# Kernel tuning notes

Measured on AMD Instinct MI355X. Metric: run time of the kernel, lower is better.

## Reference

```python
import jax, jax.numpy as jnp
import numpy as np

D_MODEL, D_STATE, D_CONV, D_INNER, DT_RANK = 96, 16, 3, 192, 6
BATCH, H, W = 4, 64, 64


def setup_inputs() -> dict:
    key = jax.random.key(0)
    ks = jax.random.split(key, 8)
    s = 0.02
    return {
        "x": jax.random.normal(ks[0], (BATCH, H, W, D_MODEL), jnp.float32),
        "in_proj_w": jax.random.normal(ks[1], (2 * D_INNER, D_MODEL), jnp.float32) * s,
        "conv_w": jax.random.normal(ks[2], (D_INNER, 1, D_CONV, D_CONV), jnp.float32) * s,
        "conv_b": jnp.zeros((D_INNER,), jnp.float32),
        "x_proj_w": jax.random.normal(ks[3], (4, DT_RANK + 2 * D_STATE, D_INNER), jnp.float32) * s,
        "dt_w": jax.random.normal(ks[4], (4, D_INNER, DT_RANK), jnp.float32) * s,
        # dt bias ~ inverse-softplus of dt in [1e-3, 1e-1] (roughly log-uniform negative values)
        "dt_b": jax.random.uniform(ks[5], (4, D_INNER), jnp.float32, minval=-6.0, maxval=-2.3),
        "A_logs": jnp.log(jnp.tile(jnp.arange(1, D_STATE + 1, dtype=jnp.float32), (4 * D_INNER, 1))),
        "Ds": jnp.ones((4 * D_INNER,), jnp.float32),
        "ln_w": jnp.ones((D_INNER,), jnp.float32),
        "ln_b": jnp.zeros((D_INNER,), jnp.float32),
        "out_proj_w": jax.random.normal(ks[6], (D_MODEL, D_INNER), jnp.float32) * s,
    }


def _ss2d(x, in_proj_w, conv_w, conv_b, x_proj_w, dt_w, dt_b, A_logs, Ds, ln_w, ln_b, out_proj_w):
    B, Hh, Ww, C = x.shape
    D = conv_w.shape[0]          # d_inner
    N = A_logs.shape[1]          # d_state
    R = dt_w.shape[2]            # dt_rank
    L = Hh * Ww
    K = 4

    xz = x @ in_proj_w.T                          # (B,H,W,2D)
    xi, z = jnp.split(xz, 2, axis=-1)
    xc = jnp.transpose(xi, (0, 3, 1, 2))          # (B,D,H,W)
    pad = (D_CONV - 1) // 2
    xc = jax.lax.conv_general_dilated(xc, conv_w, (1, 1), ((pad, pad), (pad, pad)),
                                      feature_group_count=D)
    xc = jax.nn.silu(xc + conv_b[None, :, None, None])

    # 4 scan directions: row-major, col-major, and their reverses
    x_flat = xc.reshape(B, D, L)
    x_tr = jnp.transpose(xc, (0, 1, 3, 2)).reshape(B, D, L)
    x_hwwh = jnp.stack([x_flat, x_tr], axis=1)                     # (B,2,D,L)
    xs = jnp.concatenate([x_hwwh, jnp.flip(x_hwwh, axis=-1)], axis=1)  # (B,K,D,L)

    x_dbl = jnp.einsum('bkdl,kcd->bkcl', xs, x_proj_w)
    dts, Bs, Cs = jnp.split(x_dbl, [R, R + N], axis=2)             # (B,K,R,L),(B,K,N,L),(B,K,N,L)
    dts = jnp.einsum('bkrl,kdr->bkdl', dts, dt_w)
    delta = jax.nn.softplus(dts + dt_b[None, :, :, None])          # (B,K,D,L)
    A = -jnp.exp(A_logs).reshape(K, D, N)                          # (K,D,N)

    # sequential selective scan over L (L-first for lax.scan)
    u_seq = jnp.moveaxis(xs, -1, 0)        # (L,B,K,D)
    dt_seq = jnp.moveaxis(delta, -1, 0)    # (L,B,K,D)
    B_seq = jnp.moveaxis(Bs, -1, 0)        # (L,B,K,N)
    C_seq = jnp.moveaxis(Cs, -1, 0)        # (L,B,K,N)

    def step(h, inp):
        u_t, dt_t, B_t, C_t = inp
        h = jnp.exp(dt_t[..., None] * A) * h + (dt_t * u_t)[..., None] * B_t[:, :, None, :]
        y = jnp.einsum('bkdn,bkn->bkd', h, C_t)
        return h, y

    h0 = jnp.zeros((B, K, D, N), jnp.float32)
    _, ys = jax.lax.scan(step, h0, (u_seq, dt_seq, B_seq, C_seq))
    out_y = jnp.moveaxis(ys, 0, -1) + Ds.reshape(K, D)[None, :, :, None] * xs  # (B,K,D,L)

    y1 = out_y[:, 0]
    y2 = jnp.transpose(out_y[:, 1].reshape(B, D, Ww, Hh), (0, 1, 3, 2)).reshape(B, D, L)
    y3 = jnp.flip(out_y[:, 2], axis=-1)
    y4 = jnp.transpose(jnp.flip(out_y[:, 3], axis=-1).reshape(B, D, Ww, Hh), (0, 1, 3, 2)).reshape(B, D, L)
    y = y1 + y2 + y3 + y4                                           # (B,D,L)

    y = jnp.transpose(y, (0, 2, 1)).reshape(B, Hh, Ww, D)
    mu = y.mean(-1, keepdims=True)
    var = y.var(-1, keepdims=True)
    y = (y - mu) * jax.lax.rsqrt(var + 1e-5) * ln_w + ln_b
    y = y * jax.nn.silu(z)
    return y @ out_proj_w.T


def reference(x, in_proj_w, conv_w, conv_b, x_proj_w, dt_w, dt_b, A_logs, Ds, ln_w, ln_b, out_proj_w):
    return _ss2d(x, in_proj_w, conv_w, conv_b, x_proj_w, dt_w, dt_b, A_logs, Ds, ln_w, ln_b, out_proj_w)
```

## Files before the change

### kernel.cpp

```cpp
#include <hip/hip_runtime.h>

constexpr int BATCH = 4;
constexpr int HS    = 64;
constexpr int WSZ   = 64;
constexpr int LSEQ  = 4096;
constexpr int DM    = 96;
constexpr int DI    = 192;
constexpr int NS    = 16;
constexpr int RK    = 6;
constexpr int KD    = 4;
constexpr int NCH   = 128;
constexpr int CLEN  = 32;
constexpr int XDS   = 160;

__device__ __forceinline__ int pos_of(int k, int l) {
  switch (k & 3) {
    case 0: return l;
    case 1: return ((l & 63) << 6) | (l >> 6);
    case 2: return LSEQ - 1 - l;
    default: { int lp = LSEQ - 1 - l; return ((lp & 63) << 6) | (lp >> 6); }
  }
}

__device__ __forceinline__ float softplus_f(float s) {
  return (s > 20.f) ? s : __logf(1.f + __expf(s));
}

__launch_bounds__(256)
__global__ void transpose_w(const float* __restrict__ in, float* __restrict__ outp,
                            int R, int C_) {
  int idx = blockIdx.x * 256 + threadIdx.x;
  if (idx < R * C_) {
    int r = idx / C_, c = idx % C_;
    outp[(size_t)c * R + r] = in[idx];
  }
}

template <int NN, int KK, int TM, int KT>
__launch_bounds__(256)
__global__ void gemm_nt(const float* __restrict__ A, const float* __restrict__ BT,
                        float* __restrict__ C, int M) {
  constexpr int TN  = 64;
  constexpr int RPT = TM / 16;
  constexpr int SA  = KT + 4;
  constexpr int KQ  = KT / 4;
  __shared__ float As[TM][SA];
  __shared__ float Bs[KT][TN];
  const int t = threadIdx.x;
  const int row0 = blockIdx.y * TM;
  const int col0 = blockIdx.x * TN;
  const int tc = t & 15;
  const int tr = t >> 4;

  float acc[RPT][4];
  #pragma unroll
  for (int i = 0; i < RPT; ++i)
    { acc[i][0]=0.f; acc[i][1]=0.f; acc[i][2]=0.f; acc[i][3]=0.f; }

  for (int k0 = 0; k0 < KK; k0 += KT) {
    #pragma unroll 1
    for (int idx = t; idx < TM * KQ; idx += 256) {
      int r = idx / KQ, kq = idx % KQ;
      *(float4*)&As[r][kq * 4] =
          *(const float4*)&A[(size_t)(row0 + r) * KK + k0 + kq * 4];
    }
    #pragma unroll 1
    for (int idx = t; idx < KT * 16; idx += 256) {
      int kk = idx >> 4, cq = idx & 15;
      int col = col0 + cq * 4;
      float4 v = make_float4(0.f, 0.f, 0.f, 0.f);
      if (col < NN) v = *(const float4*)&BT[(size_t)(k0 + kk) * NN + col];
      *(float4*)&Bs[kk][cq * 4] = v;
    }
    __syncthreads();
    #pragma unroll 4
    for (int kk = 0; kk < KT; ++kk) {
      float4 bv = *(const float4*)&Bs[kk][tc * 4];
      #pragma unroll
      for (int i = 0; i < RPT; ++i) {
        float a = As[tr * RPT + i][kk];
        acc[i][0] += a * bv.x; acc[i][1] += a * bv.y;
        acc[i][2] += a * bv.z; acc[i][3] += a * bv.w;
      }
    }
    __syncthreads();
  }
  int c = col0 + tc * 4;
  if (c < NN) {
    #pragma unroll
    for (int i = 0; i < RPT; ++i) {
      size_t r0 = (size_t)(row0 + tr * RPT + i) * NN + c;
      *(float4*)&C[r0] = make_float4(acc[i][0], acc[i][1], acc[i][2], acc[i][3]);
    }
  }
}

__launch_bounds__(256)
__global__ void conv_silu(const float* __restrict__ xz, const float* __restrict__ cw,
                          const float* __restrict__ cb, float* __restrict__ xc) {
  int idx = blockIdx.x * 256 + threadIdx.x;
  int d = idx % DI;
  int p = (idx / DI) % LSEQ;
  int b = idx / (DI * LSEQ);
  int h = p >> 6, w = p & 63;
  float acc = cb[d];
  #pragma unroll
  for (int kh = 0; kh < 3; ++kh) {
    int hh = h + kh - 1;
    if ((unsigned)hh >= (unsigned)HS) continue;
    #pragma unroll
    for (int kw = 0; kw < 3; ++kw) {
      int ww = w + kw - 1;
      if ((unsigned)ww >= (unsigned)WSZ) continue;
      acc += xz[((size_t)b * LSEQ + (hh << 6) + ww) * (2 * DI) + d] * cw[d * 9 + kh * 3 + kw];
    }
  }
  xc[idx] = acc / (1.f + __expf(-acc));
}

__launch_bounds__(256)
__global__ void build_wcatT(const float* __restrict__ xw, float* __restrict__ WcatT) {
  int idx = blockIdx.x * 256 + threadIdx.x;
  int col = idx / XDS, j = idx % XDS;
  int k = j / 40, jj = j % 40;
  float v = 0.f;
  int src = -1;
  if (jj < 16)      src = k * 38 + 6 + jj;
  else if (jj < 32) src = k * 38 + 22 + (jj - 16);
  else if (jj < 38) src = k * 38 + (jj - 32);
  if (src >= 0) v = xw[(size_t)src * DI + col];
  WcatT[idx] = v;
}

__launch_bounds__(192)
__global__ void scan_phase1(const float* __restrict__ xc, const float* __restrict__ xdbl,
                            const float* __restrict__ Alog, const float* __restrict__ dtw,
                            const float* __restrict__ dtb,
                            float* __restrict__ hN, float* __restrict__ sumdB) {
  const int d = threadIdx.x;
  const int ch = blockIdx.x, k = blockIdx.y, b = blockIdx.z;
  const int bk = b * KD + k;
  __shared__ float4 Bsh[CLEN * 6];
  {
    int idx = d;
    int j = idx / 6, q = idx % 6;
    int p = pos_of(k, ch * CLEN + j);
    int qq = (q < 4) ? q : (q + 4);
    Bsh[idx] = *(const float4*)&xdbl[(size_t)(b * LSEQ + p) * XDS + k * 40 + qq * 4];
  }
  float An[NS];
  {
    const float4* Ap = (const float4*)&Alog[((size_t)k * DI + d) * NS];
    #pragma unroll
    for (int q = 0; q < 4; ++q) {
      float4 a = Ap[q];
      An[q*4+0] = -__expf(a.x); An[q*4+1] = -__expf(a.y);
      An[q*4+2] = -__expf(a.z); An[q*4+3] = -__expf(a.w);
    }
  }
  float w[RK];
  #pragma unroll
  for (int r = 0; r < RK; ++r) w[r] = dtw[((size_t)k * DI + d) * RK + r];
  const float bsv = dtb[k * DI + d];
  const float An0 = An[0];
  bool geo = true;
  #pragma unroll
  for (int n = 0; n < NS; ++n)
    geo = geo && (fabsf(An[n] - (n + 1) * An0) <= 1e-3f * fabsf(An[n]));
  __syncthreads();

  float h[NS];
  #pragma unroll
  for (int n = 0; n < NS; ++n) h[n] = 0.f;
  float sumd = 0.f;
  const int l0 = ch * CLEN;
  if (geo) {
    #pragma unroll 2
    for (int j = 0; j < CLEN; ++j) {
      const int p = pos_of(k, l0 + j);
      const size_t bp = (size_t)b * LSEQ + p;
      float4 t0 = Bsh[j * 6 + 4], t1 = Bsh[j * 6 + 5];
      float s = bsv + w[0]*t0.x + w[1]*t0.y + w[2]*t0.z + w[3]*t0.w + w[4]*t1.x + w[5]*t1.y;
      float dl = softplus_f(s);
      float du = dl * xc[bp * DI + d];
      float we = __expf(dl * An0), wp = 1.f;
      #pragma unroll
      for (int q = 0; q < 4; ++q) {
        float4 v = Bsh[j * 6 + q];
        wp *= we; h[q*4+0] = wp * h[q*4+0] + du * v.x;
        wp *= we; h[q*4+1] = wp * h[q*4+1] + du * v.y;
        wp *= we; h[q*4+2] = wp * h[q*4+2] + du * v.z;
        wp *= we; h[q*4+3] = wp * h[q*4+3] + du * v.w;
      }
      sumd += dl;
    }
  } else {
    #pragma unroll 1
    for (int j = 0; j < CLEN; ++j) {
      const int p = pos_of(k, l0 + j);
      const size_t bp = (size_t)b * LSEQ + p;
      float4 t0 = Bsh[j * 6 + 4], t1 = Bsh[j * 6 + 5];
      float s = bsv + w[0]*t0.x + w[1]*t0.y + w[2]*t0.z + w[3]*t0.w + w[4]*t1.x + w[5]*t1.y;
      float dl = softplus_f(s);
      float du = dl * xc[bp * DI + d];
      #pragma unroll
      for (int q = 0; q < 4; ++q) {
        float4 v = Bsh[j * 6 + q];
        h[q*4+0] = __expf(dl * An[q*4+0]) * h[q*4+0] + du * v.x;
        h[q*4+1] = __expf(dl * An[q*4+1]) * h[q*4+1] + du * v.y;
        h[q*4+2] = __expf(dl * An[q*4+2]) * h[q*4+2] + du * v.z;
        h[q*4+3] = __expf(dl * An[q*4+3]) * h[q*4+3] + du * v.w;
      }
      sumd += dl;
    }
  }
  const size_t o = ((size_t)bk * NCH + ch) * DI + d;
  float4* Hp = (float4*)&hN[o * NS];
  #pragma unroll
  for (int q = 0; q < 4; ++q)
    Hp[q] = make_float4(h[q*4+0], h[q*4+1], h[q*4+2], h[q*4+3]);
  sumdB[o] = sumd;
}

__launch_bounds__(256)
__global__ void chunk_combine(float* __restrict__ hN, const float* __restrict__ sumdB,
                              const float* __restrict__ Alog) {
  const int tid = blockIdx.x * 256 + threadIdx.x;
  const int n  = tid & 15;
  const int dd = tid >> 4;
  const int d  = dd % DI;
  const int bk = dd / DI;
  const int k  = bk & 3;
  const float An = -__expf(Alog[((size_t)k * DI + d) * NS + n]);
  float h = 0.f;
  #pragma unroll 1
  for (int c = 0; c < NCH; ++c) {
    const size_t o = ((size_t)bk * NCH + c) * DI + d;
    float tmp = hN[o * NS + n];
    hN[o * NS + n] = h;
    h = tmp + __expf(An * sumdB[o]) * h;
  }
}

__launch_bounds__(192)
__global__ void scan_phase2(const float* __restrict__ xc, const float* __restrict__ xdbl,
                            const float* __restrict__ Alog, const float* __restrict__ dtw,
                            const float* __restrict__ dtb, const float* __restrict__ hin,
                            float* __restrict__ yg) {
  const int d = threadIdx.x;
  const int ch = blockIdx.x, k = blockIdx.y, b = blockIdx.z;
  const int bk = b * KD + k;
  __shared__ float4 Bsh[CLEN * 10];
  #pragma unroll 1
  for (int idx = d; idx < CLEN * 10; idx += 192) {
    int j = idx / 10, q = idx % 10;
    int p = pos_of(k, ch * CLEN + j);
    Bsh[idx] = *(const float4*)&xdbl[(size_t)(b * LSEQ + p) * XDS + k * 40 + q * 4];
  }
  float An[NS];
  {
    const float4* Ap = (const float4*)&Alog[((size_t)k * DI + d) * NS];
    #pragma unroll
    for (int q = 0; q < 4; ++q) {
      float4 a = Ap[q];
      An[q*4+0] = -__expf(a.x); An[q*4+1] = -__expf(a.y);
      An[q*4+2] = -__expf(a.z); An[q*4+3] = -__expf(a.w);
    }
  }
  float w[RK];
  #pragma unroll
  for (int r = 0; r < RK; ++r) w[r] = dtw[((size_t)k * DI + d) * RK + r];
  const float bsv = dtb[k * DI + d];
  const float An0 = An[0];
  bool geo = true;
  #pragma unroll
  for (int n = 0; n < NS; ++n)
    geo = geo && (fabsf(An[n] - (n + 1) * An0) <= 1e-3f * fabsf(An[n]));

  float h[NS];
  {
    const size_t o = ((size_t)bk * NCH + ch) * DI + d;
    const float4* Hp = (const float4*)&hin[o * NS];
    #pragma unroll
    for (int q = 0; q < 4; ++q) {
      float4 v = Hp[q];
      h[q*4+0] = v.x; h[q*4+1] = v.y; h[q*4+2] = v.z; h[q*4+3] = v.w;
    }
  }
  __syncthreads();
  const int l0 = ch * CLEN;
  if (geo) {
    #pragma unroll 2
    for (int j = 0; j < CLEN; ++j) {
      const int p = pos_of(k, l0 + j);
      const size_t bp = (size_t)b * LSEQ + p;
      float4 t0 = Bsh[j * 10 + 8], t1 = Bsh[j * 10 + 9];
      float s = bsv + w[0]*t0.x + w[1]*t0.y + w[2]*t0.z + w[3]*t0.w + w[4]*t1.x + w[5]*t1.y;
      float dl = softplus_f(s);
      float du = dl * xc[bp * DI + d];
      float we = __expf(dl * An0), wp = 1.f;
      float y = 0.f;
      #pragma unroll
      for (int q = 0; q < 4; ++q) {
        float4 v  = Bsh[j * 10 + q];
        float4 c4 = Bsh[j * 10 + 4 + q];
        wp *= we; h[q*4+0] = wp * h[q*4+0] + du * v.x; y += h[q*4+0] * c4.x;
        wp *= we; h[q*4+1] = wp * h[q*4+1] + du * v.y; y += h[q*4+1] * c4.y;
        wp *= we; h[q*4+2] = wp * h[q*4+2] + du * v.z; y += h[q*4+2] * c4.z;
        wp *= we; h[q*4+3] = wp * h[q*4+3] + du * v.w; y += h[q*4+3] * c4.w;
      }
      atomicAdd(&yg[bp * DI + d], y);
    }
  } else {
    #pragma unroll 1
    for (int j = 0; j < CLEN; ++j) {
      const int p = pos_of(k, l0 + j);
      const size_t bp = (size_t)b * LSEQ + p;
      float4 t0 = Bsh[j * 10 + 8], t1 = Bsh[j * 10 + 9];
      float s = bsv + w[0]*t0.x + w[1]*t0.y + w[2]*t0.z + w[3]*t0.w + w[4]*t1.x + w[5]*t1.y;
      float dl = softplus_f(s);
      float du = dl * xc[bp * DI + d];
      float y = 0.f;
      #pragma unroll
      for (int q = 0; q < 4; ++q) {
        float4 v  = Bsh[j * 10 + q];
        float4 c4 = Bsh[j * 10 + 4 + q];
        h[q*4+0] = __expf(dl * An[q*4+0]) * h[q*4+0] + du * v.x; y += h[q*4+0] * c4.x;
        h[q*4+1] = __expf(dl * An[q*4+1]) * h[q*4+1] + du * v.y; y += h[q*4+1] * c4.y;
        h[q*4+2] = __expf(dl * An[q*4+2]) * h[q*4+2] + du * v.z; y += h[q*4+2] * c4.z;
        h[q*4+3] = __expf(dl * An[q*4+3]) * h[q*4+3] + du * v.w; y += h[q*4+3] * c4.w;
      }
      atomicAdd(&yg[bp * DI + d], y);
    }
  }
}

__launch_bounds__(192)
__global__ void fuse_ln(const float* __restrict__ yg, const float* __restrict__ xc,
                        const float* __restrict__ Ds, const float* __restrict__ xz,
                        const float* __restrict__ lnw, const float* __restrict__ lnb,
                        float* __restrict__ ymul) {
  const int row = blockIdx.x;
  const int d = threadIdx.x;
  float u = xc[(size_t)row * DI + d];
  float sDs = Ds[d] + Ds[DI + d] + Ds[2 * DI + d] + Ds[3 * DI + d];
  float y = yg[(size_t)row * DI + d] + sDs * u;
  float s1 = y, s2 = y * y;
  #pragma unroll
  for (int off = 32; off; off >>= 1) {
    s1 += __shfl_xor(s1, off);
    s2 += __shfl_xor(s2, off);
  }
  __shared__ float r1[3], r2[3];
  int wid = d >> 6;
  if ((d & 63) == 0) { r1[wid] = s1; r2[wid] = s2; }
  __syncthreads();
  float S1 = r1[0] + r1[1] + r1[2];
  float S2 = r2[0] + r2[1] + r2[2];
  float mu = S1 * (1.f / DI);
  float var = S2 * (1.f / DI) - mu * mu;
  float yn = (y - mu) * rsqrtf(var + 1e-5f) * lnw[d] + lnb[d];
  float zv = xz[(size_t)row * (2 * DI) + DI + d];
  float g = zv / (1.f + __expf(-zv));
  ymul[(size_t)row * DI + d] = yn * g;
}

extern "C" void kernel_launch(void* const* d_in, const int* in_sizes, int n_in,
                              void* d_out, int out_size, void* d_ws, size_t ws_size,
                              hipStream_t stream) {
  (void)in_sizes; (void)n_in; (void)out_size; (void)ws_size;
  const float* x          = (const float*)d_in[0];
  const float* in_proj_w  = (const float*)d_in[1];
  const float* conv_w     = (const float*)d_in[2];
  const float* conv_b     = (const float*)d_in[3];
  const float* x_proj_w   = (const float*)d_in[4];
  const float* dt_w       = (const float*)d_in[5];
  const float* dt_b       = (const float*)d_in[6];
  const float* A_logs     = (const float*)d_in[7];
  const float* Ds         = (const float*)d_in[8];
  const float* ln_w       = (const float*)d_in[9];
  const float* ln_b       = (const float*)d_in[10];
  const float* out_proj_w = (const float*)d_in[11];
  float* out = (float*)d_out;
  float* ws  = (float*)d_ws;

  constexpr size_t SZ_XZ    = (size_t)BATCH * LSEQ * 2 * DI;
  constexpr size_t SZ_XC    = (size_t)BATCH * LSEQ * DI;
  constexpr size_t SZ_XD    = (size_t)BATCH * LSEQ * XDS;
  constexpr size_t SZ_HN    = (size_t)BATCH * KD * NCH * DI * NS;
  constexpr size_t SZ_SUMD  = (size_t)BATCH * KD * NCH * DI;

  float* xz    = ws;
  float* xc    = xz + SZ_XZ;
  float* xdbl  = xc + SZ_XC;
  float* hN    = xdbl + SZ_XD;
  float* sumd  = hN + SZ_HN;
  float* yg    = sumd + SZ_SUMD;
  float* ymul  = yg + SZ_XC;
  float* WcatT = ymul + SZ_XC;
  float* inpT  = WcatT + (size_t)DI * XDS;
  float* outpT = inpT + (size_t)DM * 2 * DI;

  const int M = BATCH * LSEQ;

  build_wcatT<<<(DI * XDS) / 256, 256, 0, stream>>>(x_proj_w, WcatT);
  transpose_w<<<(2 * DI * DM + 255) / 256, 256, 0, stream>>>(in_proj_w, inpT, 2 * DI, DM);
  transpose_w<<<(DM * DI + 255) / 256, 256, 0, stream>>>(out_proj_w, outpT, DM, DI);
  gemm_nt<2 * DI, DM, 64, 96><<<dim3(6, M / 64), 256, 0, stream>>>(x, inpT, xz, M);
  conv_silu<<<(BATCH * LSEQ * DI) / 256, 256, 0, stream>>>(xz, conv_w, conv_b, xc);
  gemm_nt<XDS, DI, 64, 96><<<dim3(3, M / 64), 256, 0, stream>>>(xc, WcatT, xdbl, M);
  scan_phase1<<<dim3(NCH, KD, BATCH), 192, 0, stream>>>(xc, xdbl, A_logs, dt_w, dt_b,
                                                        hN, sumd);
  chunk_combine<<<(BATCH * KD * DI * NS) / 256, 256, 0, stream>>>(hN, sumd, A_logs);
  hipMemsetAsync(yg, 0, SZ_XC * sizeof(float), stream);
  scan_phase2<<<dim3(NCH, KD, BATCH), 192, 0, stream>>>(xc, xdbl, A_logs, dt_w, dt_b,
                                                        hN, yg);
  fuse_ln<<<M, DI, 0, stream>>>(yg, xc, Ds, xz, ln_w, ln_b, ymul);
  gemm_nt<DM, DI, 64, 96><<<dim3(2, M / 64), 256, 0, stream>>>(ymul, outpT, out, M);
}
```

Baseline: 236.3 us.

## Compute intra-chunk outputs in phase 1 and add carry-in correction in phase 2

Phase 1 now runs the full zero-initial-state chunk scan, producing y contributions and the chunk-final states in one pass. Phase 2 no longer repeats the recurrence. It adds only the carried-in state's contribution, scaled by the cumulative decay exp(A*cumsum(dt)) projected onto C, and skips chunk 0 entirely. Decay powers in the geometric-A path are also built with a short power tree instead of a serial multiply chain. The cost is extra atomic adds in phase 1 and possible precision differences from large cumulative-decay exponents.

```diff
diff --git a/kernel.cpp b/kernel.cpp
--- a/kernel.cpp
+++ b/kernel.cpp
@@ -24,6 +24,14 @@
 
 __device__ __forceinline__ float softplus_f(float s) {
   return (s > 20.f) ? s : __logf(1.f + __expf(s));
+}
+
+__device__ __forceinline__ void pw16(float e, float* p) {
+  float e2 = e * e, e4 = e2 * e2, e8 = e4 * e4;
+  p[1] = e;       p[2] = e2;      p[3] = e2 * e;  p[4] = e4;
+  p[5] = e4 * e;  p[6] = e4 * e2; p[7] = p[6] * e; p[8] = e8;
+  p[9] = e8 * e;  p[10] = e8 * e2; p[11] = p[10] * e; p[12] = e8 * e4;
+  p[13] = p[12] * e; p[14] = p[12] * e2; p[15] = p[14] * e; p[16] = e8 * e8;
 }
 
 __launch_bounds__(256)
@@ -136,116 +144,7 @@
 __global__ void scan_phase1(const float* __restrict__ xc, const float* __restrict__ xdbl,
                             const float* __restrict__ Alog, const float* __restrict__ dtw,
                             const float* __restrict__ dtb,
-                            float* __restrict__ hN, float* __restrict__ sumdB) {
-  const int d = threadIdx.x;
-  const int ch = blockIdx.x, k = blockIdx.y, b = blockIdx.z;
-  const int bk = b * KD + k;
-  __shared__ float4 Bsh[CLEN * 6];
-  {
-    int idx = d;
-    int j = idx / 6, q = idx % 6;
-    int p = pos_of(k, ch * CLEN + j);
-    int qq = (q < 4) ? q : (q + 4);
-    Bsh[idx] = *(const float4*)&xdbl[(size_t)(b * LSEQ + p) * XDS + k * 40 + qq * 4];
-  }
-  float An[NS];
-  {
-    const float4* Ap = (const float4*)&Alog[((size_t)k * DI + d) * NS];
-    #pragma unroll
-    for (int q = 0; q < 4; ++q) {
-      float4 a = Ap[q];
-      An[q*4+0] = -__expf(a.x); An[q*4+1] = -__expf(a.y);
-      An[q*4+2] = -__expf(a.z); An[q*4+3] = -__expf(a.w);
-    }
-  }
-  float w[RK];
-  #pragma unroll
-  for (int r = 0; r < RK; ++r) w[r] = dtw[((size_t)k * DI + d) * RK + r];
-  const float bsv = dtb[k * DI + d];
-  const float An0 = An[0];
-  bool geo = true;
-  #pragma unroll
-  for (int n = 0; n < NS; ++n)
-    geo = geo && (fabsf(An[n] - (n + 1) * An0) <= 1e-3f * fabsf(An[n]));
-  __syncthreads();
-
-  float h[NS];
-  #pragma unroll
-  for (int n = 0; n < NS; ++n) h[n] = 0.f;
-  float sumd = 0.f;
-  const int l0 = ch * CLEN;
-  if (geo) {
-    #pragma unroll 2
-    for (int j = 0; j < CLEN; ++j) {
-      const int p = pos_of(k, l0 + j);
-      const size_t bp = (size_t)b * LSEQ + p;
-      float4 t0 = Bsh[j * 6 + 4], t1 = Bsh[j * 6 + 5];
-      float s = bsv + w[0]*t0.x + w[1]*t0.y + w[2]*t0.z + w[3]*t0.w + w[4]*t1.x + w[5]*t1.y;
-      float dl = softplus_f(s);
-      float du = dl * xc[bp * DI + d];
-      float we = __expf(dl * An0), wp = 1.f;
-      #pragma unroll
-      for (int q = 0; q < 4; ++q) {
-        float4 v = Bsh[j * 6 + q];
-        wp *= we; h[q*4+0] = wp * h[q*4+0] + du * v.x;
-        wp *= we; h[q*4+1] = wp * h[q*4+1] + du * v.y;
-        wp *= we; h[q*4+2] = wp * h[q*4+2] + du * v.z;
-        wp *= we; h[q*4+3] = wp * h[q*4+3] + du * v.w;
-      }
-      sumd += dl;
-    }
-  } else {
-    #pragma unroll 1
-    for (int j = 0; j < CLEN; ++j) {
-      const int p = pos_of(k, l0 + j);
-      const size_t bp = (size_t)b * LSEQ + p;
-      float4 t0 = Bsh[j * 6 + 4], t1 = Bsh[j * 6 + 5];
-      float s = bsv + w[0]*t0.x + w[1]*t0.y + w[2]*t0.z + w[3]*t0.w + w[4]*t1.x + w[5]*t1.y;
-      float dl = softplus_f(s);
-      float du = dl * xc[bp * DI + d];
-      #pragma unroll
-      for (int q = 0; q < 4; ++q) {
-        float4 v = Bsh[j * 6 + q];
-        h[q*4+0] = __expf(dl * An[q*4+0]) * h[q*4+0] + du * v.x;
-        h[q*4+1] = __expf(dl * An[q*4+1]) * h[q*4+1] + du * v.y;
-        h[q*4+2] = __expf(dl * An[q*4+2]) * h[q*4+2] + du * v.z;
-        h[q*4+3] = __expf(dl * An[q*4+3]) * h[q*4+3] + du * v.w;
-      }
-      sumd += dl;
-    }
-  }
-  const size_t o = ((size_t)bk * NCH + ch) * DI + d;
-  float4* Hp = (float4*)&hN[o * NS];
-  #pragma unroll
-  for (int q = 0; q < 4; ++q)
-    Hp[q] = make_float4(h[q*4+0], h[q*4+1], h[q*4+2], h[q*4+3]);
-  sumdB[o] = sumd;
-}
-
-__launch_bounds__(256)
-__global__ void chunk_combine(float* __restrict__ hN, const float* __restrict__ sumdB,
-                              const float* __restrict__ Alog) {
-  const int tid = blockIdx.x * 256 + threadIdx.x;
-  const int n  = tid & 15;
-  const int dd = tid >> 4;
-  const int d  = dd % DI;
-  const int bk = dd / DI;
-  const int k  = bk & 3;
-  const float An = -__expf(Alog[((size_t)k * DI + d) * NS + n]);
-  float h = 0.f;
-  #pragma unroll 1
-  for (int c = 0; c < NCH; ++c) {
-    const size_t o = ((size_t)bk * NCH + c) * DI + d;
-    float tmp = hN[o * NS + n];
-    hN[o * NS + n] = h;
-    h = tmp + __expf(An * sumdB[o]) * h;
-  }
-}
-
-__launch_bounds__(192)
-__global__ void scan_phase2(const float* __restrict__ xc, const float* __restrict__ xdbl,
-                            const float* __restrict__ Alog, const float* __restrict__ dtw,
-                            const float* __restrict__ dtb, const float* __restrict__ hin,
+                            float* __restrict__ hN, float* __restrict__ sumdB,
                             float* __restrict__ yg) {
   const int d = threadIdx.x;
   const int ch = blockIdx.x, k = blockIdx.y, b = blockIdx.z;
@@ -276,18 +175,12 @@
   #pragma unroll
   for (int n = 0; n < NS; ++n)
     geo = geo && (fabsf(An[n] - (n + 1) * An0) <= 1e-3f * fabsf(An[n]));
+  __syncthreads();
 
   float h[NS];
-  {
-    const size_t o = ((size_t)bk * NCH + ch) * DI + d;
-    const float4* Hp = (const float4*)&hin[o * NS];
-    #pragma unroll
-    for (int q = 0; q < 4; ++q) {
-      float4 v = Hp[q];
-      h[q*4+0] = v.x; h[q*4+1] = v.y; h[q*4+2] = v.z; h[q*4+3] = v.w;
-    }
-  }
-  __syncthreads();
+  #pragma unroll
+  for (int n = 0; n < NS; ++n) h[n] = 0.f;
+  float sumd = 0.f;
   const int l0 = ch * CLEN;
   if (geo) {
     #pragma unroll 2
@@ -298,17 +191,19 @@
       float s = bsv + w[0]*t0.x + w[1]*t0.y + w[2]*t0.z + w[3]*t0.w + w[4]*t1.x + w[5]*t1.y;
       float dl = softplus_f(s);
       float du = dl * xc[bp * DI + d];
-      float we = __expf(dl * An0), wp = 1.f;
+      float pw[17];
+      pw16(__expf(dl * An0), pw);
       float y = 0.f;
       #pragma unroll
       for (int q = 0; q < 4; ++q) {
         float4 v  = Bsh[j * 10 + q];
         float4 c4 = Bsh[j * 10 + 4 + q];
-        wp *= we; h[q*4+0] = wp * h[q*4+0] + du * v.x; y += h[q*4+0] * c4.x;
-        wp *= we; h[q*4+1] = wp * h[q*4+1] + du * v.y; y += h[q*4+1] * c4.y;
-        wp *= we; h[q*4+2] = wp * h[q*4+2] + du * v.z; y += h[q*4+2] * c4.z;
-        wp *= we; h[q*4+3] = wp * h[q*4+3] + du * v.w; y += h[q*4+3] * c4.w;
+        h[q*4+0] = pw[q*4+1] * h[q*4+0] + du * v.x; y += h[q*4+0] * c4.x;
+        h[q*4+1] = pw[q*4+2] * h[q*4+1] + du * v.y; y += h[q*4+1] * c4.y;
+        h[q*4+2] = pw[q*4+3] * h[q*4+2] + du * v.z; y += h[q*4+2] * c4.z;
+        h[q*4+3] = pw[q*4+4] * h[q*4+3] + du * v.w; y += h[q*4+3] * c4.w;
       }
+      sumd += dl;
       atomicAdd(&yg[bp * DI + d], y);
     }
   } else {
@@ -330,6 +225,125 @@
         h[q*4+2] = __expf(dl * An[q*4+2]) * h[q*4+2] + du * v.z; y += h[q*4+2] * c4.z;
         h[q*4+3] = __expf(dl * An[q*4+3]) * h[q*4+3] + du * v.w; y += h[q*4+3] * c4.w;
       }
+      sumd += dl;
+      atomicAdd(&yg[bp * DI + d], y);
+    }
+  }
+  const size_t o = ((size_t)bk * NCH + ch) * DI + d;
+  float4* Hp = (float4*)&hN[o * NS];
+  #pragma unroll
+  for (int q = 0; q < 4; ++q)
+    Hp[q] = make_float4(h[q*4+0], h[q*4+1], h[q*4+2], h[q*4+3]);
+  sumdB[o] = sumd;
+}
+
+__launch_bounds__(256)
+__global__ void chunk_combine(float* __restrict__ hN, const float* __restrict__ sumdB,
+                              const float* __restrict__ Alog) {
+  const int tid = blockIdx.x * 256 + threadIdx.x;
+  const int n  = tid & 15;
+  const int dd = tid >> 4;
+  const int d  = dd % DI;
+  const int bk = dd / DI;
+  const int k  = bk & 3;
+  const float An = -__expf(Alog[((size_t)k * DI + d) * NS + n]);
+  float h = 0.f;
+  #pragma unroll 1
+  for (int c = 0; c < NCH; ++c) {
+    const size_t o = ((size_t)bk * NCH + c) * DI + d;
+    float tmp = hN[o * NS + n];
+    hN[o * NS + n] = h;
+    h = tmp + __expf(An * sumdB[o]) * h;
+  }
+}
+
+__launch_bounds__(192)
+__global__ void scan_phase2(const float* __restrict__ xdbl, const float* __restrict__ Alog,
+                            const float* __restrict__ dtw, const float* __restrict__ dtb,
+                            const float* __restrict__ hin, float* __restrict__ yg) {
+  const int ch = blockIdx.x;
+  if (ch == 0) return;
+  const int d = threadIdx.x;
+  const int k = blockIdx.y, b = blockIdx.z;
+  const int bk = b * KD + k;
+  __shared__ float4 Bsh[CLEN * 6];
+  {
+    int idx = d;
+    int j = idx / 6, q = idx % 6;
+    int p = pos_of(k, ch * CLEN + j);
+    Bsh[idx] = *(const float4*)&xdbl[(size_t)(b * LSEQ + p) * XDS + k * 40 + (q + 4) * 4];
+  }
+  float An[NS];
+  {
+    const float4* Ap = (const float4*)&Alog[((size_t)k * DI + d) * NS];
+    #pragma unroll
+    for (int q = 0; q < 4; ++q) {
+      float4 a = Ap[q];
+      An[q*4+0] = -__expf(a.x); An[q*4+1] = -__expf(a.y);
+      An[q*4+2] = -__expf(a.z); An[q*4+3] = -__expf(a.w);
+    }
+  }
+  float w[RK];
+  #pragma unroll
+  for (int r = 0; r < RK; ++r) w[r] = dtw[((size_t)k * DI + d) * RK + r];
+  const float bsv = dtb[k * DI + d];
+  const float An0 = An[0];
+  bool geo = true;
+  #pragma unroll
+  for (int n = 0; n < NS; ++n)
+    geo = geo && (fabsf(An[n] - (n + 1) * An0) <= 1e-3f * fabsf(An[n]));
+
+  float g[NS];
+  {
+    const size_t o = ((size_t)bk * NCH + ch) * DI + d;
+    const float4* Hp = (const float4*)&hin[o * NS];
+    #pragma unroll
+    for (int q = 0; q < 4; ++q) {
+      float4 v = Hp[q];
+      g[q*4+0] = v.x; g[q*4+1] = v.y; g[q*4+2] = v.z; g[q*4+3] = v.w;
+    }
+  }
+  __syncthreads();
+  const int l0 = ch * CLEN;
+  float cum = 0.f;
+  if (geo) {
+    #pragma unroll 2
+    for (int j = 0; j < CLEN; ++j) {
+      const int p = pos_of(k, l0 + j);
+      const size_t bp = (size_t)b * LSEQ + p;
+      float4 t0 = Bsh[j * 6 + 4], t1 = Bsh[j * 6 + 5];
+      float s = bsv + w[0]*t0.x + w[1]*t0.y + w[2]*t0.z + w[3]*t0.w + w[4]*t1.x + w[5]*t1.y;
+      cum += softplus_f(s);
+      float pw[17];
+      pw16(__expf(cum * An0), pw);
+      float y = 0.f;
+      #pragma unroll
+      for (int q = 0; q < 4; ++q) {
+        float4 c4 = Bsh[j * 6 + q];
+        y += (pw[q*4+1] * g[q*4+0]) * c4.x;
+        y += (pw[q*4+2] * g[q*4+1]) * c4.y;
+        y += (pw[q*4+3] * g[q*4+2]) * c4.z;
+        y += (pw[q*4+4] * g[q*4+3]) * c4.w;
+      }
+      atomicAdd(&yg[bp * DI + d], y);
+    }
+  } else {
+    #pragma unroll 1
+    for (int j = 0; j < CLEN; ++j) {
+      const int p = pos_of(k, l0 + j);
+      const size_t bp = (size_t)b * LSEQ + p;
+      float4 t0 = Bsh[j * 6 + 4], t1 = Bsh[j * 6 + 5];
+      float s = bsv + w[0]*t0.x + w[1]*t0.y + w[2]*t0.z + w[3]*t0.w + w[4]*t1.x + w[5]*t1.y;
+      cum += softplus_f(s);
+      float y = 0.f;
+      #pragma unroll
+      for (int q = 0; q < 4; ++q) {
+        float4 c4 = Bsh[j * 6 + q];
+        y += (__expf(An[q*4+0] * cum) * g[q*4+0]) * c4.x;
+        y += (__expf(An[q*4+1] * cum) * g[q*4+1]) * c4.y;
+        y += (__expf(An[q*4+2] * cum) * g[q*4+2]) * c4.z;
+        y += (__expf(An[q*4+3] * cum) * g[q*4+3]) * c4.w;
+      }
       atomicAdd(&yg[bp * DI + d], y);
     }
   }
@@ -409,12 +423,11 @@
   gemm_nt<2 * DI, DM, 64, 96><<<dim3(6, M / 64), 256, 0, stream>>>(x, inpT, xz, M);
   conv_silu<<<(BATCH * LSEQ * DI) / 256, 256, 0, stream>>>(xz, conv_w, conv_b, xc);
   gemm_nt<XDS, DI, 64, 96><<<dim3(3, M / 64), 256, 0, stream>>>(xc, WcatT, xdbl, M);
+  hipMemsetAsync(yg, 0, SZ_XC * sizeof(float), stream);
   scan_phase1<<<dim3(NCH, KD, BATCH), 192, 0, stream>>>(xc, xdbl, A_logs, dt_w, dt_b,
-                                                        hN, sumd);
+                                                        hN, sumd, yg);
   chunk_combine<<<(BATCH * KD * DI * NS) / 256, 256, 0, stream>>>(hN, sumd, A_logs);
-  hipMemsetAsync(yg, 0, SZ_XC * sizeof(float), stream);
-  scan_phase2<<<dim3(NCH, KD, BATCH), 192, 0, stream>>>(xc, xdbl, A_logs, dt_w, dt_b,
-                                                        hN, yg);
+  scan_phase2<<<dim3(NCH, KD, BATCH), 192, 0, stream>>>(xdbl, A_logs, dt_w, dt_b, hN, yg);
   fuse_ln<<<M, DI, 0, stream>>>(yg, xc, Ds, xz, ln_w, ln_b, ymul);
   gemm_nt<DM, DI, 64, 96><<<dim3(2, M / 64), 256, 0, stream>>>(ymul, outpT, out, M);
 }
```

Result: slower. 252.5 us (+6.9%).

## Write per-direction scan outputs to planes instead of atomics, sum in LN

Applied to the files above, without the earlier changes.

scan_phase2 now writes each direction's y into its own plane with plain stores instead of atomicAdd into a shared buffer, and fuse_ln sums the four planes. This removes the memset and the atomic contention at the cost of four times the intermediate storage and extra reads in fuse_ln. The serial power chain wp*=we is replaced by a log-depth power computation (pw16) to shorten the dependency chain. The geometric check now compares A_logs directly against log(n+1) offsets.

```diff
diff --git a/kernel.cpp b/kernel.cpp
--- a/kernel.cpp
+++ b/kernel.cpp
@@ -24,6 +24,26 @@
 
 __device__ __forceinline__ float softplus_f(float s) {
   return (s > 20.f) ? s : __logf(1.f + __expf(s));
+}
+
+__device__ __forceinline__ void pw16(float e, float* p) {
+  float e2 = e * e, e4 = e2 * e2, e8 = e4 * e4;
+  p[1] = e;       p[2] = e2;      p[3] = e2 * e;  p[4] = e4;
+  p[5] = e4 * e;  p[6] = e4 * e2; p[7] = p[6] * e; p[8] = e8;
+  p[9] = e8 * e;  p[10] = e8 * e2; p[11] = p[10] * e; p[12] = e8 * e4;
+  p[13] = p[12] * e; p[14] = p[12] * e2; p[15] = p[14] * e; p[16] = e8 * e8;
+}
+
+__device__ __forceinline__ bool geo_check(const float* Al) {
+  const float lntab[16] = {0.f, 0.6931472f, 1.0986123f, 1.3862944f, 1.6094379f,
+                           1.7917595f, 1.9459101f, 2.0794415f, 2.1972246f, 2.3025851f,
+                           2.3978953f, 2.4849066f, 2.5649494f, 2.6390573f, 2.7080502f,
+                           2.7725887f};
+  bool g = true;
+  #pragma unroll
+  for (int n = 0; n < NS; ++n)
+    g = g && (fabsf(Al[n] - Al[0] - lntab[n]) <= 2e-3f);
+  return g;
 }
 
 __launch_bounds__(256)
@@ -148,25 +168,21 @@
     int qq = (q < 4) ? q : (q + 4);
     Bsh[idx] = *(const float4*)&xdbl[(size_t)(b * LSEQ + p) * XDS + k * 40 + qq * 4];
   }
-  float An[NS];
+  float Al[NS];
   {
     const float4* Ap = (const float4*)&Alog[((size_t)k * DI + d) * NS];
     #pragma unroll
     for (int q = 0; q < 4; ++q) {
       float4 a = Ap[q];
-      An[q*4+0] = -__expf(a.x); An[q*4+1] = -__expf(a.y);
-      An[q*4+2] = -__expf(a.z); An[q*4+3] = -__expf(a.w);
-    }
-  }
+      Al[q*4+0] = a.x; Al[q*4+1] = a.y; Al[q*4+2] = a.z; Al[q*4+3] = a.w;
+    }
+  }
+  const bool geo = geo_check(Al);
+  const float An0 = -__expf(Al[0]);
   float w[RK];
   #pragma unroll
   for (int r = 0; r < RK; ++r) w[r] = dtw[((size_t)k * DI + d) * RK + r];
   const float bsv = dtb[k * DI + d];
-  const float An0 = An[0];
-  bool geo = true;
-  #pragma unroll
-  for (int n = 0; n < NS; ++n)
-    geo = geo && (fabsf(An[n] - (n + 1) * An0) <= 1e-3f * fabsf(An[n]));
   __syncthreads();
 
   float h[NS];
@@ -183,18 +199,22 @@
       float s = bsv + w[0]*t0.x + w[1]*t0.y + w[2]*t0.z + w[3]*t0.w + w[4]*t1.x + w[5]*t1.y;
       float dl = softplus_f(s);
       float du = dl * xc[bp * DI + d];
-      float we = __expf(dl * An0), wp = 1.f;
+      float pw[17];
+      pw16(__expf(dl * An0), pw);
       #pragma unroll
       for (int q = 0; q < 4; ++q) {
         float4 v = Bsh[j * 6 + q];
-        wp *= we; h[q*4+0] = wp * h[q*4+0] + du * v.x;
-        wp *= we; h[q*4+1] = wp * h[q*4+1] + du * v.y;
-        wp *= we; h[q*4+2] = wp * h[q*4+2] + du * v.z;
-        wp *= we; h[q*4+3] = wp * h[q*4+3] + du * v.w;
+        h[q*4+0] = pw[q*4+1] * h[q*4+0] + du * v.x;
+        h[q*4+1] = pw[q*4+2] * h[q*4+1] + du * v.y;
+        h[q*4+2] = pw[q*4+3] * h[q*4+2] + du * v.z;
+        h[q*4+3] = pw[q*4+4] * h[q*4+3] + du * v.w;
       }
       sumd += dl;
     }
   } else {
+    float An[NS];
+    #pragma unroll
+    for (int n = 0; n < NS; ++n) An[n] = -__expf(Al[n]);
     #pragma unroll 1
     for (int j = 0; j < CLEN; ++j) {
       const int p = pos_of(k, l0 + j);
@@ -246,7 +266,7 @@
 __global__ void scan_phase2(const float* __restrict__ xc, const float* __restrict__ xdbl,
                             const float* __restrict__ Alog, const float* __restrict__ dtw,
                             const float* __restrict__ dtb, const float* __restrict__ hin,
-                            float* __restrict__ yg) {
+                            float* __restrict__ ypl) {
   const int d = threadIdx.x;
   const int ch = blockIdx.x, k = blockIdx.y, b = blockIdx.z;
   const int bk = b * KD + k;
@@ -257,25 +277,21 @@
     int p = pos_of(k, ch * CLEN + j);
     Bsh[idx] = *(const float4*)&xdbl[(size_t)(b * LSEQ + p) * XDS + k * 40 + q * 4];
   }
-  float An[NS];
+  float Al[NS];
   {
     const float4* Ap = (const float4*)&Alog[((size_t)k * DI + d) * NS];
     #pragma unroll
     for (int q = 0; q < 4; ++q) {
       float4 a = Ap[q];
-      An[q*4+0] = -__expf(a.x); An[q*4+1] = -__expf(a.y);
-      An[q*4+2] = -__expf(a.z); An[q*4+3] = -__expf(a.w);
-    }
-  }
+      Al[q*4+0] = a.x; Al[q*4+1] = a.y; Al[q*4+2] = a.z; Al[q*4+3] = a.w;
+    }
+  }
+  const bool geo = geo_check(Al);
+  const float An0 = -__expf(Al[0]);
   float w[RK];
   #pragma unroll
   for (int r = 0; r < RK; ++r) w[r] = dtw[((size_t)k * DI + d) * RK + r];
   const float bsv = dtb[k * DI + d];
-  const float An0 = An[0];
-  bool geo = true;
-  #pragma unroll
-  for (int n = 0; n < NS; ++n)
-    geo = geo && (fabsf(An[n] - (n + 1) * An0) <= 1e-3f * fabsf(An[n]));
 
   float h[NS];
   {
@@ -288,6 +304,7 @@
     }
   }
   __syncthreads();
+  float* yout = ypl + (size_t)bk * LSEQ * DI;
   const int l0 = ch * CLEN;
   if (geo) {
     #pragma unroll 2
@@ -298,20 +315,24 @@
       float s = bsv + w[0]*t0.x + w[1]*t0.y + w[2]*t0.z + w[3]*t0.w + w[4]*t1.x + w[5]*t1.y;
       float dl = softplus_f(s);
       float du = dl * xc[bp * DI + d];
-      float we = __expf(dl * An0), wp = 1.f;
+      float pw[17];
+      pw16(__expf(dl * An0), pw);
       float y = 0.f;
       #pragma unroll
       for (int q = 0; q < 4; ++q) {
         float4 v  = Bsh[j * 10 + q];
         float4 c4 = Bsh[j * 10 + 4 + q];
-        wp *= we; h[q*4+0] = wp * h[q*4+0] + du * v.x; y += h[q*4+0] * c4.x;
-        wp *= we; h[q*4+1] = wp * h[q*4+1] + du * v.y; y += h[q*4+1] * c4.y;
-        wp *= we; h[q*4+2] = wp * h[q*4+2] + du * v.z; y += h[q*4+2] * c4.z;
-        wp *= we; h[q*4+3] = wp * h[q*4+3] + du * v.w; y += h[q*4+3] * c4.w;
+        h[q*4+0] = pw[q*4+1] * h[q*4+0] + du * v.x; y += h[q*4+0] * c4.x;
+        h[q*4+1] = pw[q*4+2] * h[q*4+1] + du * v.y; y += h[q*4+1] * c4.y;
+        h[q*4+2] = pw[q*4+3] * h[q*4+2] + du * v.z; y += h[q*4+2] * c4.z;
+        h[q*4+3] = pw[q*4+4] * h[q*4+3] + du * v.w; y += h[q*4+3] * c4.w;
       }
-      atomicAdd(&yg[bp * DI + d], y);
+      yout[(size_t)p * DI + d] = y;
     }
   } else {
+    float An[NS];
+    #pragma unroll
+    for (int n = 0; n < NS; ++n) An[n] = -__expf(Al[n]);
     #pragma unroll 1
     for (int j = 0; j < CLEN; ++j) {
       const int p = pos_of(k, l0 + j);
@@ -330,21 +351,25 @@
         h[q*4+2] = __expf(dl * An[q*4+2]) * h[q*4+2] + du * v.z; y += h[q*4+2] * c4.z;
         h[q*4+3] = __expf(dl * An[q*4+3]) * h[q*4+3] + du * v.w; y += h[q*4+3] * c4.w;
       }
-      atomicAdd(&yg[bp * DI + d], y);
+      yout[(size_t)p * DI + d] = y;
     }
   }
 }
 
 __launch_bounds__(192)
-__global__ void fuse_ln(const float* __restrict__ yg, const float* __restrict__ xc,
+__global__ void fuse_ln(const float* __restrict__ ypl, const float* __restrict__ xc,
                         const float* __restrict__ Ds, const float* __restrict__ xz,
                         const float* __restrict__ lnw, const float* __restrict__ lnb,
                         float* __restrict__ ymul) {
   const int row = blockIdx.x;
+  const int b = row >> 12;
+  const size_t pd = (size_t)row * DI + threadIdx.x;
   const int d = threadIdx.x;
-  float u = xc[(size_t)row * DI + d];
+  constexpr size_t PL = (size_t)LSEQ * DI;
+  float u = xc[pd];
   float sDs = Ds[d] + Ds[DI + d] + Ds[2 * DI + d] + Ds[3 * DI + d];
-  float y = yg[(size_t)row * DI + d] + sDs * u;
+  const size_t base = (size_t)(b * KD) * PL + pd - (size_t)b * PL;
+  float y = ypl[base] + ypl[base + PL] + ypl[base + 2 * PL] + ypl[base + 3 * PL] + sDs * u;
   float s1 = y, s2 = y * y;
   #pragma unroll
   for (int off = 32; off; off >>= 1) {
@@ -362,7 +387,7 @@
   float yn = (y - mu) * rsqrtf(var + 1e-5f) * lnw[d] + lnb[d];
   float zv = xz[(size_t)row * (2 * DI) + DI + d];
   float g = zv / (1.f + __expf(-zv));
-  ymul[(size_t)row * DI + d] = yn * g;
+  ymul[pd] = yn * g;
 }
 
 extern "C" void kernel_launch(void* const* d_in, const int* in_sizes, int n_in,
@@ -389,14 +414,15 @@
   constexpr size_t SZ_XD    = (size_t)BATCH * LSEQ * XDS;
   constexpr size_t SZ_HN    = (size_t)BATCH * KD * NCH * DI * NS;
   constexpr size_t SZ_SUMD  = (size_t)BATCH * KD * NCH * DI;
+  constexpr size_t SZ_YPL   = (size_t)BATCH * KD * LSEQ * DI;
 
   float* xz    = ws;
   float* xc    = xz + SZ_XZ;
   float* xdbl  = xc + SZ_XC;
   float* hN    = xdbl + SZ_XD;
   float* sumd  = hN + SZ_HN;
-  float* yg    = sumd + SZ_SUMD;
-  float* ymul  = yg + SZ_XC;
+  float* ypl   = sumd + SZ_SUMD;
+  float* ymul  = ypl + SZ_YPL;
   float* WcatT = ymul + SZ_XC;
   float* inpT  = WcatT + (size_t)DI * XDS;
   float* outpT = inpT + (size_t)DM * 2 * DI;
@@ -412,9 +438,8 @@
   scan_phase1<<<dim3(NCH, KD, BATCH), 192, 0, stream>>>(xc, xdbl, A_logs, dt_w, dt_b,
                                                         hN, sumd);
   chunk_combine<<<(BATCH * KD * DI * NS) / 256, 256, 0, stream>>>(hN, sumd, A_logs);
-  hipMemsetAsync(yg, 0, SZ_XC * sizeof(float), stream);
   scan_phase2<<<dim3(NCH, KD, BATCH), 192, 0, stream>>>(xc, xdbl, A_logs, dt_w, dt_b,
-                                                        hN, yg);
-  fuse_ln<<<M, DI, 0, stream>>>(yg, xc, Ds, xz, ln_w, ln_b, ymul);
+                                                        hN, ypl);
+  fuse_ln<<<M, DI, 0, stream>>>(ypl, xc, Ds, xz, ln_w, ln_b, ymul);
   gemm_nt<DM, DI, 64, 96><<<dim3(2, M / 64), 256, 0, stream>>>(ymul, outpT, out, M);
 }
```

Measured after the change: 233.7 us. About the same (-1.1%).
